# Kernel optimization log

Hardware: AMD Instinct MI355X
Metric: run time of the kernel (lower is better)

Reference implementation:

```python
import jax, jax.numpy as jnp
import numpy as np

D_MODEL = 1024
N_HEAD = 16
B, C, S = 4, 4, 1024


def setup_inputs() -> dict:
    key = jax.random.key(0)
    ks = jax.random.split(key, 5)
    d = D_MODEL
    x = jax.random.normal(ks[0], (B, C, S, d), dtype=jnp.float32)
    scale = 1.0 / np.sqrt(d).astype(np.float32)

    def lin(k):
        return jax.random.normal(k, (d, d), dtype=jnp.float32) * scale

    return {
        "x": x,
        "wq": lin(ks[1]), "bq": jnp.zeros((d,), jnp.float32),
        "wk": lin(ks[2]), "bk": jnp.zeros((d,), jnp.float32),
        "wv": lin(ks[3]), "bv": jnp.zeros((d,), jnp.float32),
        "wo": lin(ks[4]), "bo": jnp.zeros((d,), jnp.float32),
    }


def reference(x, wq, bq, wk, bk, wv, bv, wo, bo):
    b, c, s, d = x.shape
    dh = d // N_HEAD
    nh = N_HEAD * c  # channels folded into heads, as in torch .view

    def proj(w, bias):
        # nn.Linear: y = x @ w.T + b  (w stored as [out, in])
        y = jnp.einsum('bcsd,ed->bcse', x, w) + bias
        # view(B, -1, n_head*C, d_head).transpose(1, 2) -> (B, nh, S, dh)
        return jnp.swapaxes(y.reshape(b, -1, nh, dh), 1, 2)

    # NOTE: original multiplies query by sqrt(d_head) (kept faithfully)
    q = proj(wq, bq) * jnp.sqrt(jnp.asarray(dh, x.dtype))
    k = proj(wk, bk)
    v = proj(wv, bv)

    attn = jax.nn.softmax(jnp.einsum('bhqd,bhkd->bhqk', q, k), axis=-1)
    o = jnp.einsum('bhqk,bhkd->bhqd', attn, v)          # (B, nh, S, dh)
    o = jnp.swapaxes(o, 1, 2).reshape(b, -1, N_HEAD * dh)  # (B, S*C, d)
    o = jnp.einsum('bnd,ed->bne', o, wo) + bo
    return o.reshape(b, c, -1, d)  # (B, C, S, d)
```

## Files before the change

kernel.cpp:

```cpp
#include <hip/hip_runtime.h>
#include <stdint.h>

typedef unsigned short u16;
typedef _Float16 f16;
typedef __attribute__((ext_vector_type(8))) _Float16 f16x8;
typedef __attribute__((ext_vector_type(4))) float f32x4;

__device__ __forceinline__ float exp2fast(float x) {
  return __builtin_amdgcn_exp2f(x);
}

__device__ __forceinline__ f32x4 mfma16(f16x8 a, f16x8 b, f32x4 c) {
  return __builtin_amdgcn_mfma_f32_16x16x32_f16(a, b, c, 0, 0, 0);
}

__device__ __forceinline__ u16 f2h(float f) {
  return __builtin_bit_cast(u16, (f16)f);
}

__device__ __forceinline__ void gld16(const void* g, void* l) {
  __builtin_amdgcn_global_load_lds(
      (const __attribute__((address_space(1))) unsigned int*)g,
      (__attribute__((address_space(3))) unsigned int*)l,
      16, 0, 0);
}

__global__ __launch_bounds__(256) void cvt_f32_f16(const float* __restrict__ in,
                                                   u16* __restrict__ out, int n4) {
  int stride = gridDim.x * blockDim.x;
  for (int i = blockIdx.x * blockDim.x + threadIdx.x; i < n4; i += stride) {
    float4 v = reinterpret_cast<const float4*>(in)[i];
    ushort4 o;
    o.x = f2h(v.x); o.y = f2h(v.y); o.z = f2h(v.z); o.w = f2h(v.w);
    reinterpret_cast<ushort4*>(out)[i] = o;
  }
}

struct Ptr8 {
  const float *s0, *s1, *s2, *s3;
  u16 *d0, *d1, *d2, *d3;
};
__global__ __launch_bounds__(256) void cvt4_f32_f16(Ptr8 p, int n4) {
  const float* in = (blockIdx.y == 0) ? p.s0 : (blockIdx.y == 1) ? p.s1
                    : (blockIdx.y == 2) ? p.s2 : p.s3;
  u16* out = (blockIdx.y == 0) ? p.d0 : (blockIdx.y == 1) ? p.d1
             : (blockIdx.y == 2) ? p.d2 : p.d3;
  int stride = gridDim.x * blockDim.x;
  for (int i = blockIdx.x * blockDim.x + threadIdx.x; i < n4; i += stride) {
    float4 v = reinterpret_cast<const float4*>(in)[i];
    ushort4 o;
    o.x = f2h(v.x); o.y = f2h(v.y); o.z = f2h(v.z); o.w = f2h(v.w);
    reinterpret_cast<ushort4*>(out)[i] = o;
  }
}

__device__ __forceinline__ void stage64(const u16* __restrict__ M, int r0, int k0,
                                        u16* S, int wid, int lane) {
  const int l8 = lane >> 3;
  const int col = k0 + (((lane & 7) ^ l8) << 3);
#pragma unroll
  for (int it = 0; it < 4; ++it) {
    const int rowbase = wid * 32 + it * 8;
    gld16(M + (size_t)(r0 + rowbase + l8) * 1024 + col, S + rowbase * 64);
  }
}

__global__ __launch_bounds__(256) void proj_qkv(
    const u16* __restrict__ xb,
    const u16* __restrict__ wqh, const u16* __restrict__ wkh, const u16* __restrict__ wvh,
    const float* __restrict__ bq, const float* __restrict__ bk, const float* __restrict__ bv,
    u16* __restrict__ Qf, u16* __restrict__ Kf, u16* __restrict__ Vt) {
  const int mat = blockIdx.z;
  const u16* __restrict__ w = (mat == 0) ? wqh : (mat == 1) ? wkh : wvh;
  const float* __restrict__ bias = (mat == 0) ? bq : (mat == 1) ? bk : bv;
  const int m0 = blockIdx.x * 128;
  const int n0 = blockIdx.y * 128;

  __shared__ __align__(16) u16 As[128 * 64];
  __shared__ __align__(16) u16 Bs[128 * 64];

  const int tid = threadIdx.x;
  const int lane = tid & 63;
  const int wid = tid >> 6;
  const int wr = wid >> 1, wc = wid & 1;
  const int qd = lane >> 4, lm = lane & 15;

  f32x4 acc[4][4];
#pragma unroll
  for (int i = 0; i < 4; ++i)
#pragma unroll
    for (int j = 0; j < 4; ++j) acc[i][j] = (f32x4){0.f, 0.f, 0.f, 0.f};

  stage64(xb, m0, 0, As, wid, lane);
  stage64(w, n0, 0, Bs, wid, lane);

  for (int kt = 0; kt < 16; ++kt) {
    __syncthreads();
#pragma unroll
    for (int ks = 0; ks < 2; ++ks) {
      const int gofs = ((ks * 4 + qd) ^ (lm & 7)) << 3;
      f16x8 af[4], bf[4];
#pragma unroll
      for (int i = 0; i < 4; ++i)
        af[i] = *reinterpret_cast<const f16x8*>(As + (wr * 64 + i * 16 + lm) * 64 + gofs);
#pragma unroll
      for (int j = 0; j < 4; ++j)
        bf[j] = *reinterpret_cast<const f16x8*>(Bs + (wc * 64 + j * 16 + lm) * 64 + gofs);
#pragma unroll
      for (int i = 0; i < 4; ++i)
#pragma unroll
        for (int j = 0; j < 4; ++j)
          acc[i][j] = mfma16(af[i], bf[j], acc[i][j]);
    }
    __syncthreads();
    if (kt + 1 < 16) {
      stage64(xb, m0, (kt + 1) * 64, As, wid, lane);
      stage64(w, n0, (kt + 1) * 64, Bs, wid, lane);
    }
  }

  const float scale = (mat == 0) ? 11.5415603f : 1.0f;
#pragma unroll
  for (int i = 0; i < 4; ++i) {
#pragma unroll
    for (int r = 0; r < 4; ++r) {
      int R = m0 + wr * 64 + i * 16 + qd * 4 + r;
      int bb = R >> 12, n = R & 4095;
      int cc = n >> 10, s = n & 1023;
      int rb = s & 3, t = s >> 2;
      int m = cc * 256 + t;
#pragma unroll
      for (int j = 0; j < 4; ++j) {
        int e = n0 + wc * 64 + j * 16 + lm;
        int head = e >> 6, jj = e & 63;
        int h = rb * 16 + head;
        float val = (acc[i][j][r] + bias[e]) * scale;
        u16 hv = f2h(val);
        if (mat == 2) {
          Vt[(((size_t)bb * 64 + h) * 64 + jj) * 1024 + m] = hv;
        } else {
          size_t idx = (((size_t)bb * 64 + h) * 1024 + m) * 64 + jj;
          if (mat == 0) Qf[idx] = hv;
          else          Kf[idx] = hv;
        }
      }
    }
  }
}

__device__ __forceinline__ f16x8 lds_frag(const u16* base, int row, int blk) {
  return *reinterpret_cast<const f16x8*>(base + row * 64 + ((blk ^ (row & 7)) << 3));
}

__device__ __forceinline__ void stage_kv(const u16* __restrict__ Kh,
                                         const u16* __restrict__ Vh, int kc,
                                         u16* KsB, u16* VsB, int wv, int lane) {
  const int l8 = lane >> 3, sl = lane & 7;
  const int rb = wv * 16;
#pragma unroll
  for (int it = 0; it < 2; ++it) {
    int row = rb + it * 8 + l8;
    int gsl = sl ^ l8;
    gld16(Kh + (size_t)(kc * 64 + row) * 64 + gsl * 8, KsB + (rb + it * 8) * 64);
    gld16(Vh + (size_t)row * 1024 + kc * 64 + gsl * 8, VsB + (rb + it * 8) * 64);
  }
}

__global__ __launch_bounds__(256) void attn_kernel(
    const u16* __restrict__ Qf, const u16* __restrict__ Kf,
    const u16* __restrict__ Vt, u16* __restrict__ Of) {
  const int wgid = (blockIdx.x & 7) * 256 + (blockIdx.x >> 3);
  const int bh = wgid >> 3;
  const int m0 = (wgid & 7) * 128;
  const int b = bh >> 6, h = bh & 63;
  const int tid = threadIdx.x, lane = tid & 63, wv = tid >> 6;
  const int qd = lane >> 4, lm = lane & 15;

  __shared__ __align__(16) u16 Ks[2][64 * 64];
  __shared__ __align__(16) u16 Vs[2][64 * 64];

  const size_t hb = (size_t)(b * 64 + h);
  const u16* __restrict__ Qh = Qf + hb * 65536;
  const u16* __restrict__ Kh = Kf + hb * 65536;
  const u16* __restrict__ Vh = Vt + hb * 65536;

  f16x8 qf[2][2];
#pragma unroll
  for (int im = 0; im < 2; ++im)
#pragma unroll
    for (int ks = 0; ks < 2; ++ks)
      qf[im][ks] = *reinterpret_cast<const f16x8*>(
          Qh + (size_t)(m0 + wv * 32 + im * 16 + lm) * 64 + ks * 32 + qd * 8);

  f32x4 oa[2][4];
  float mrow[2] = {-1e30f, -1e30f};
  float lrow[2] = {0.f, 0.f};
#pragma unroll
  for (int im = 0; im < 2; ++im)
#pragma unroll
    for (int jf = 0; jf < 4; ++jf) oa[im][jf] = (f32x4){0.f, 0.f, 0.f, 0.f};

  stage_kv(Kh, Vh, 0, &Ks[0][0], &Vs[0][0], wv, lane);

  for (int kc = 0; kc < 16; ++kc) {
    const int buf = kc & 1;
    __syncthreads();
    if (kc + 1 < 16) stage_kv(Kh, Vh, kc + 1, &Ks[buf ^ 1][0], &Vs[buf ^ 1][0], wv, lane);

    f32x4 sc[2][4];
#pragma unroll
    for (int im = 0; im < 2; ++im)
#pragma unroll
      for (int nf = 0; nf < 4; ++nf) sc[im][nf] = (f32x4){0.f, 0.f, 0.f, 0.f};
    __builtin_amdgcn_s_setprio(1);
#pragma unroll
    for (int ks = 0; ks < 2; ++ks) {
      f16x8 kfr[4];
#pragma unroll
      for (int nf = 0; nf < 4; ++nf)
        kfr[nf] = lds_frag(&Ks[buf][0], nf * 16 + lm, ks * 4 + qd);
#pragma unroll
      for (int im = 0; im < 2; ++im)
#pragma unroll
        for (int nf = 0; nf < 4; ++nf)
          sc[im][nf] = mfma16(kfr[nf], qf[im][ks], sc[im][nf]);
    }
    __builtin_amdgcn_s_setprio(0);

    unsigned int pk[2][8];
#pragma unroll
    for (int im = 0; im < 2; ++im) {
      float pm = sc[im][0][0];
#pragma unroll
      for (int nf = 0; nf < 4; ++nf)
#pragma unroll
        for (int r = 0; r < 4; ++r) pm = fmaxf(pm, sc[im][nf][r]);
      pm = fmaxf(pm, __shfl_xor(pm, 16));
      pm = fmaxf(pm, __shfl_xor(pm, 32));
      if (__all(pm <= mrow[im] + 8.0f)) {
        float mn = mrow[im];
        float s = 0.f;
#pragma unroll
        for (int nf = 0; nf < 4; ++nf) {
          float p0 = exp2fast(sc[im][nf][0] - mn);
          float p1 = exp2fast(sc[im][nf][1] - mn);
          float p2 = exp2fast(sc[im][nf][2] - mn);
          float p3 = exp2fast(sc[im][nf][3] - mn);
          s += (p0 + p1) + (p2 + p3);
          pk[im][2 * nf + 0] = __builtin_bit_cast(unsigned int, __builtin_amdgcn_cvt_pkrtz(p0, p1));
          pk[im][2 * nf + 1] = __builtin_bit_cast(unsigned int, __builtin_amdgcn_cvt_pkrtz(p2, p3));
        }
        s += __shfl_xor(s, 16);
        s += __shfl_xor(s, 32);
        lrow[im] += s;
      } else {
        float mn = fmaxf(mrow[im], pm);
        float corr = exp2fast(mrow[im] - mn);
        mrow[im] = mn;
        float s = 0.f;
#pragma unroll
        for (int nf = 0; nf < 4; ++nf) {
          float p0 = exp2fast(sc[im][nf][0] - mn);
          float p1 = exp2fast(sc[im][nf][1] - mn);
          float p2 = exp2fast(sc[im][nf][2] - mn);
          float p3 = exp2fast(sc[im][nf][3] - mn);
          s += (p0 + p1) + (p2 + p3);
          pk[im][2 * nf + 0] = __builtin_bit_cast(unsigned int, __builtin_amdgcn_cvt_pkrtz(p0, p1));
          pk[im][2 * nf + 1] = __builtin_bit_cast(unsigned int, __builtin_amdgcn_cvt_pkrtz(p2, p3));
        }
        s += __shfl_xor(s, 16);
        s += __shfl_xor(s, 32);
        lrow[im] = lrow[im] * corr + s;
#pragma unroll
        for (int r = 0; r < 4; ++r) {
          float cb = __shfl(corr, qd * 4 + r);
#pragma unroll
          for (int jf = 0; jf < 4; ++jf) oa[im][jf][r] *= cb;
        }
      }
    }

#pragma unroll
    for (int ks = 0; ks < 2; ++ks) {
      f16x8 vfr[4];
#pragma unroll
      for (int jf = 0; jf < 4; ++jf)
        vfr[jf] = lds_frag(&Vs[buf][0], jf * 16 + lm, ks * 4 + qd);
#pragma unroll
      for (int im = 0; im < 2; ++im) {
        union { unsigned int w[4]; f16x8 hv; } pa;
#pragma unroll
        for (int w = 0; w < 4; ++w) {
          int srcl = (((2 * qd + (w >> 1)) & 3) << 4) + lm;
          unsigned int a0 = __shfl(pk[im][2 * (2 * ks + 0) + (w & 1)], srcl);
          unsigned int a1 = __shfl(pk[im][2 * (2 * ks + 1) + (w & 1)], srcl);
          pa.w[w] = (qd & 2) ? a1 : a0;
        }
        __builtin_amdgcn_s_setprio(1);
#pragma unroll
        for (int jf = 0; jf < 4; ++jf)
          oa[im][jf] = mfma16(pa.hv, vfr[jf], oa[im][jf]);
        __builtin_amdgcn_s_setprio(0);
      }
    }
  }

  const int rb = h >> 4, head = h & 15;
#pragma unroll
  for (int im = 0; im < 2; ++im) {
#pragma unroll
    for (int r = 0; r < 4; ++r) {
      float lb = __shfl(lrow[im], qd * 4 + r);
      float inv = 1.0f / lb;
      int mq = m0 + wv * 32 + im * 16 + qd * 4 + r;
      int c = mq >> 8, t = mq & 255;
      int s = t * 4 + rb;
      int n = c * 1024 + s;
#pragma unroll
      for (int jf = 0; jf < 4; ++jf) {
        int j = jf * 16 + lm;
        int f = head * 64 + j;
        Of[((size_t)b * 4096 + n) * 1024 + f] = f2h(oa[im][jf][r] * inv);
      }
    }
  }
}

__global__ __launch_bounds__(256) void out_gemm(
    const u16* __restrict__ Of, const u16* __restrict__ woh,
    const float* __restrict__ bo, float* __restrict__ out) {
  const int m0 = blockIdx.x * 128;
  const int n0 = blockIdx.y * 128;

  __shared__ __align__(16) u16 As[128 * 64];
  __shared__ __align__(16) u16 Bs[128 * 64];

  const int tid = threadIdx.x;
  const int lane = tid & 63;
  const int wid = tid >> 6;
  const int wr = wid >> 1, wc = wid & 1;
  const int qd = lane >> 4, lm = lane & 15;

  f32x4 acc[4][4];
#pragma unroll
  for (int i = 0; i < 4; ++i)
#pragma unroll
    for (int j = 0; j < 4; ++j) acc[i][j] = (f32x4){0.f, 0.f, 0.f, 0.f};

  stage64(Of, m0, 0, As, wid, lane);
  stage64(woh, n0, 0, Bs, wid, lane);

  for (int kt = 0; kt < 16; ++kt) {
    __syncthreads();
#pragma unroll
    for (int ks = 0; ks < 2; ++ks) {
      const int gofs = ((ks * 4 + qd) ^ (lm & 7)) << 3;
      f16x8 af[4], bf[4];
#pragma unroll
      for (int i = 0; i < 4; ++i)
        af[i] = *reinterpret_cast<const f16x8*>(As + (wr * 64 + i * 16 + lm) * 64 + gofs);
#pragma unroll
      for (int j = 0; j < 4; ++j)
        bf[j] = *reinterpret_cast<const f16x8*>(Bs + (wc * 64 + j * 16 + lm) * 64 + gofs);
#pragma unroll
      for (int i = 0; i < 4; ++i)
#pragma unroll
        for (int j = 0; j < 4; ++j)
          acc[i][j] = mfma16(af[i], bf[j], acc[i][j]);
    }
    __syncthreads();
    if (kt + 1 < 16) {
      stage64(Of, m0, (kt + 1) * 64, As, wid, lane);
      stage64(woh, n0, (kt + 1) * 64, Bs, wid, lane);
    }
  }

#pragma unroll
  for (int i = 0; i < 4; ++i) {
#pragma unroll
    for (int r = 0; r < 4; ++r) {
      int R = m0 + wr * 64 + i * 16 + qd * 4 + r;
#pragma unroll
      for (int j = 0; j < 4; ++j) {
        int e = n0 + wc * 64 + j * 16 + lm;
        out[(size_t)R * 1024 + e] = acc[i][j][r] + bo[e];
      }
    }
  }
}

extern "C" void kernel_launch(void* const* d_in, const int* in_sizes, int n_in,
                              void* d_out, int out_size, void* d_ws, size_t ws_size,
                              hipStream_t stream) {
  const float* x  = (const float*)d_in[0];
  const float* wq = (const float*)d_in[1];
  const float* bq = (const float*)d_in[2];
  const float* wk = (const float*)d_in[3];
  const float* bk = (const float*)d_in[4];
  const float* wv = (const float*)d_in[5];
  const float* bv = (const float*)d_in[6];
  const float* wo = (const float*)d_in[7];
  const float* bo = (const float*)d_in[8];
  float* out = (float*)d_out;

  char* ws = (char*)d_ws;
  u16* xb  = (u16*)(ws + 0);
  u16* wqh = (u16*)(ws + 33554432);
  u16* wkh = (u16*)(ws + 35651584);
  u16* wvh = (u16*)(ws + 37748736);
  u16* woh = (u16*)(ws + 39845888);
  u16* Qfb = (u16*)(ws + 41943040);
  u16* Kfb = (u16*)(ws + 75497472);
  u16* Vtb = (u16*)(ws + 109051904);
  u16* Ofb = (u16*)(ws + 142606336);

  cvt_f32_f16<<<4096, 256, 0, stream>>>(x, xb, 16777216 / 4);
  Ptr8 p { wq, wk, wv, wo, wqh, wkh, wvh, woh };
  cvt4_f32_f16<<<dim3(256, 4), 256, 0, stream>>>(p, 1048576 / 4);

  proj_qkv<<<dim3(128, 8, 3), 256, 0, stream>>>(xb, wqh, wkh, wvh, bq, bk, bv,
                                                Qfb, Kfb, Vtb);
  attn_kernel<<<2048, 256, 0, stream>>>(Qfb, Kfb, Vtb, Ofb);
  out_gemm<<<dim3(128, 8), 256, 0, stream>>>(Ofb, woh, bo, out);
}
```

Before: 384.4 us.

## Triple-buffer GEMM LDS staging with K=32 tiles and vmcnt-based barriers

The projection and output GEMMs move from a single-buffered K=64 tile loop, with two __syncthreads per step, to a three-stage ring of K=32 tiles. Each stage is issued two steps ahead through global_load_lds and waited on with s_waitcnt vmcnt plus a single barrier. The goal is to overlap global-to-LDS loads with MFMA work instead of stalling at each barrier. In exchange, shared memory use grows from 32KB to 48KB per block, which may lower occupancy, and the LDS swizzle changes to fit the new row width.

```diff
diff --git a/kernel.cpp b/kernel.cpp
--- a/kernel.cpp
+++ b/kernel.cpp
@@ -24,6 +24,8 @@
       (__attribute__((address_space(3))) unsigned int*)l,
       16, 0, 0);
 }
+
+#define WAITBAR(N) asm volatile("s_waitcnt vmcnt(" #N ")\n\ts_barrier" ::: "memory")
 
 __global__ __launch_bounds__(256) void cvt_f32_f16(const float* __restrict__ in,
                                                    u16* __restrict__ out, int n4) {
@@ -54,15 +56,12 @@
   }
 }
 
-__device__ __forceinline__ void stage64(const u16* __restrict__ M, int r0, int k0,
+__device__ __forceinline__ void stage32(const u16* __restrict__ M, int r0, int k0,
                                         u16* S, int wid, int lane) {
-  const int l8 = lane >> 3;
-  const int col = k0 + (((lane & 7) ^ l8) << 3);
-#pragma unroll
-  for (int it = 0; it < 4; ++it) {
-    const int rowbase = wid * 32 + it * 8;
-    gld16(M + (size_t)(r0 + rowbase + l8) * 1024 + col, S + rowbase * 64);
-  }
+  const int gr = (((lane & 3) ^ ((lane >> 3) & 3)) << 3);
+  const int row = wid * 32 + (lane >> 2);
+  gld16(M + (size_t)(r0 + row) * 1024 + k0 + gr, S + wid * 1024);
+  gld16(M + (size_t)(r0 + row + 16) * 1024 + k0 + gr, S + wid * 1024 + 512);
 }
 
 __global__ __launch_bounds__(256) void proj_qkv(
@@ -76,14 +75,15 @@
   const int m0 = blockIdx.x * 128;
   const int n0 = blockIdx.y * 128;
 
-  __shared__ __align__(16) u16 As[128 * 64];
-  __shared__ __align__(16) u16 Bs[128 * 64];
+  __shared__ __align__(16) u16 As[3 * 4096];
+  __shared__ __align__(16) u16 Bs[3 * 4096];
 
   const int tid = threadIdx.x;
   const int lane = tid & 63;
   const int wid = tid >> 6;
   const int wr = wid >> 1, wc = wid & 1;
   const int qd = lane >> 4, lm = lane & 15;
+  const int rg = (qd ^ ((lm >> 1) & 3)) << 3;
 
   f32x4 acc[4][4];
 #pragma unroll
@@ -91,32 +91,37 @@
 #pragma unroll
     for (int j = 0; j < 4; ++j) acc[i][j] = (f32x4){0.f, 0.f, 0.f, 0.f};
 
-  stage64(xb, m0, 0, As, wid, lane);
-  stage64(w, n0, 0, Bs, wid, lane);
-
-  for (int kt = 0; kt < 16; ++kt) {
-    __syncthreads();
-#pragma unroll
-    for (int ks = 0; ks < 2; ++ks) {
-      const int gofs = ((ks * 4 + qd) ^ (lm & 7)) << 3;
-      f16x8 af[4], bf[4];
-#pragma unroll
-      for (int i = 0; i < 4; ++i)
-        af[i] = *reinterpret_cast<const f16x8*>(As + (wr * 64 + i * 16 + lm) * 64 + gofs);
+  stage32(xb, m0, 0, As, wid, lane);
+  stage32(w, n0, 0, Bs, wid, lane);
+  stage32(xb, m0, 32, As + 4096, wid, lane);
+  stage32(w, n0, 32, Bs + 4096, wid, lane);
+
+  int cur = 0;
+  for (int t = 0; t < 32; ++t) {
+    if (t < 31) WAITBAR(4); else WAITBAR(0);
+
+    if (t + 2 < 32) {
+      int nb = cur + 2; if (nb >= 3) nb -= 3;
+      stage32(xb, m0, (t + 2) * 32, As + nb * 4096, wid, lane);
+      stage32(w, n0, (t + 2) * 32, Bs + nb * 4096, wid, lane);
+    }
+
+    const u16* aB = As + cur * 4096;
+    const u16* bB = Bs + cur * 4096;
+    f16x8 af[4], bf[4];
+#pragma unroll
+    for (int i = 0; i < 4; ++i)
+      af[i] = *reinterpret_cast<const f16x8*>(aB + (wr * 64 + i * 16 + lm) * 32 + rg);
+#pragma unroll
+    for (int j = 0; j < 4; ++j)
+      bf[j] = *reinterpret_cast<const f16x8*>(bB + (wc * 64 + j * 16 + lm) * 32 + rg);
+#pragma unroll
+    for (int i = 0; i < 4; ++i)
 #pragma unroll
       for (int j = 0; j < 4; ++j)
-        bf[j] = *reinterpret_cast<const f16x8*>(Bs + (wc * 64 + j * 16 + lm) * 64 + gofs);
-#pragma unroll
-      for (int i = 0; i < 4; ++i)
-#pragma unroll
-        for (int j = 0; j < 4; ++j)
-          acc[i][j] = mfma16(af[i], bf[j], acc[i][j]);
-    }
-    __syncthreads();
-    if (kt + 1 < 16) {
-      stage64(xb, m0, (kt + 1) * 64, As, wid, lane);
-      stage64(w, n0, (kt + 1) * 64, Bs, wid, lane);
-    }
+        acc[i][j] = mfma16(af[i], bf[j], acc[i][j]);
+
+    ++cur; if (cur == 3) cur = 0;
   }
 
   const float scale = (mat == 0) ? 11.5415603f : 1.0f;
@@ -332,14 +337,15 @@
   const int m0 = blockIdx.x * 128;
   const int n0 = blockIdx.y * 128;
 
-  __shared__ __align__(16) u16 As[128 * 64];
-  __shared__ __align__(16) u16 Bs[128 * 64];
+  __shared__ __align__(16) u16 As[3 * 4096];
+  __shared__ __align__(16) u16 Bs[3 * 4096];
 
   const int tid = threadIdx.x;
   const int lane = tid & 63;
   const int wid = tid >> 6;
   const int wr = wid >> 1, wc = wid & 1;
   const int qd = lane >> 4, lm = lane & 15;
+  const int rg = (qd ^ ((lm >> 1) & 3)) << 3;
 
   f32x4 acc[4][4];
 #pragma unroll
@@ -347,32 +353,34 @@
 #pragma unroll
     for (int j = 0; j < 4; ++j) acc[i][j] = (f32x4){0.f, 0.f, 0.f, 0.f};
 
-  stage64(Of, m0, 0, As, wid, lane);
-  stage64(woh, n0, 0, Bs, wid, lane);
-
-  for (int kt = 0; kt < 16; ++kt) {
-    __syncthreads();
-#pragma unroll
-    for (int ks = 0; ks < 2; ++ks) {
-      const int gofs = ((ks * 4 + qd) ^ (lm & 7)) << 3;
-      f16x8 af[4], bf[4];
-#pragma unroll
-      for (int i = 0; i < 4; ++i)
-        af[i] = *reinterpret_cast<const f16x8*>(As + (wr * 64 + i * 16 + lm) * 64 + gofs);
+  stage32(Of, m0, 0, As, wid, lane);
+  stage32(woh, n0, 0, Bs, wid, lane);
+  stage32(Of, m0, 32, As + 4096, wid, lane);
+  stage32(woh, n0, 32, Bs + 4096, wid, lane);
+
+  int cur = 0;
+  for (int t = 0; t < 32; ++t) {
+    if (t < 31) WAITBAR(4); else WAITBAR(0);
+    if (t + 2 < 32) {
+      int nb = cur + 2; if (nb >= 3) nb -= 3;
+      stage32(Of, m0, (t + 2) * 32, As + nb * 4096, wid, lane);
+      stage32(woh, n0, (t + 2) * 32, Bs + nb * 4096, wid, lane);
+    }
+    const u16* aB = As + cur * 4096;
+    const u16* bB = Bs + cur * 4096;
+    f16x8 af[4], bf[4];
+#pragma unroll
+    for (int i = 0; i < 4; ++i)
+      af[i] = *reinterpret_cast<const f16x8*>(aB + (wr * 64 + i * 16 + lm) * 32 + rg);
+#pragma unroll
+    for (int j = 0; j < 4; ++j)
+      bf[j] = *reinterpret_cast<const f16x8*>(bB + (wc * 64 + j * 16 + lm) * 32 + rg);
+#pragma unroll
+    for (int i = 0; i < 4; ++i)
 #pragma unroll
       for (int j = 0; j < 4; ++j)
-        bf[j] = *reinterpret_cast<const f16x8*>(Bs + (wc * 64 + j * 16 + lm) * 64 + gofs);
-#pragma unroll
-      for (int i = 0; i < 4; ++i)
-#pragma unroll
-        for (int j = 0; j < 4; ++j)
-          acc[i][j] = mfma16(af[i], bf[j], acc[i][j]);
-    }
-    __syncthreads();
-    if (kt + 1 < 16) {
-      stage64(Of, m0, (kt + 1) * 64, As, wid, lane);
-      stage64(woh, n0, (kt + 1) * 64, Bs, wid, lane);
-    }
+        acc[i][j] = mfma16(af[i], bf[j], acc[i][j]);
+    ++cur; if (cur == 3) cur = 0;
   }
 
 #pragma unroll
```

After: 399.6 us. 1.04x slower.

## Fuse Q/K/V projections into one block sharing the staged x tile

Applied to the files above, without the earlier changes.

Each QKV projection block now computes all three outputs (Q, K, V) for its tile. The x tile in LDS is loaded once and reused across three weight tiles, which removes two of every three loads of x and cuts the grid from 3072 to 1024 blocks. In exchange, each thread holds three times as many accumulators (192 floats) and each block uses 64KB of LDS. That can reduce occupancy or cause register spills, and fewer blocks means less parallelism across the CUs.

```diff
diff --git a/kernel.cpp b/kernel.cpp
--- a/kernel.cpp
+++ b/kernel.cpp
@@ -70,14 +70,11 @@
     const u16* __restrict__ wqh, const u16* __restrict__ wkh, const u16* __restrict__ wvh,
     const float* __restrict__ bq, const float* __restrict__ bk, const float* __restrict__ bv,
     u16* __restrict__ Qf, u16* __restrict__ Kf, u16* __restrict__ Vt) {
-  const int mat = blockIdx.z;
-  const u16* __restrict__ w = (mat == 0) ? wqh : (mat == 1) ? wkh : wvh;
-  const float* __restrict__ bias = (mat == 0) ? bq : (mat == 1) ? bk : bv;
   const int m0 = blockIdx.x * 128;
   const int n0 = blockIdx.y * 128;
 
   __shared__ __align__(16) u16 As[128 * 64];
-  __shared__ __align__(16) u16 Bs[128 * 64];
+  __shared__ __align__(16) u16 Bs[3][128 * 64];
 
   const int tid = threadIdx.x;
   const int lane = tid & 63;
@@ -85,63 +82,77 @@
   const int wr = wid >> 1, wc = wid & 1;
   const int qd = lane >> 4, lm = lane & 15;
 
-  f32x4 acc[4][4];
-#pragma unroll
-  for (int i = 0; i < 4; ++i)
-#pragma unroll
-    for (int j = 0; j < 4; ++j) acc[i][j] = (f32x4){0.f, 0.f, 0.f, 0.f};
+  f32x4 acc[3][4][4];
+#pragma unroll
+  for (int mt = 0; mt < 3; ++mt)
+#pragma unroll
+    for (int i = 0; i < 4; ++i)
+#pragma unroll
+      for (int j = 0; j < 4; ++j) acc[mt][i][j] = (f32x4){0.f, 0.f, 0.f, 0.f};
 
   stage64(xb, m0, 0, As, wid, lane);
-  stage64(w, n0, 0, Bs, wid, lane);
+  stage64(wqh, n0, 0, Bs[0], wid, lane);
+  stage64(wkh, n0, 0, Bs[1], wid, lane);
+  stage64(wvh, n0, 0, Bs[2], wid, lane);
 
   for (int kt = 0; kt < 16; ++kt) {
     __syncthreads();
 #pragma unroll
     for (int ks = 0; ks < 2; ++ks) {
       const int gofs = ((ks * 4 + qd) ^ (lm & 7)) << 3;
-      f16x8 af[4], bf[4];
+      f16x8 af[4];
 #pragma unroll
       for (int i = 0; i < 4; ++i)
         af[i] = *reinterpret_cast<const f16x8*>(As + (wr * 64 + i * 16 + lm) * 64 + gofs);
 #pragma unroll
-      for (int j = 0; j < 4; ++j)
-        bf[j] = *reinterpret_cast<const f16x8*>(Bs + (wc * 64 + j * 16 + lm) * 64 + gofs);
-#pragma unroll
-      for (int i = 0; i < 4; ++i)
+      for (int mt = 0; mt < 3; ++mt) {
+        f16x8 bf[4];
 #pragma unroll
         for (int j = 0; j < 4; ++j)
-          acc[i][j] = mfma16(af[i], bf[j], acc[i][j]);
+          bf[j] = *reinterpret_cast<const f16x8*>(Bs[mt] + (wc * 64 + j * 16 + lm) * 64 + gofs);
+#pragma unroll
+        for (int i = 0; i < 4; ++i)
+#pragma unroll
+          for (int j = 0; j < 4; ++j)
+            acc[mt][i][j] = mfma16(af[i], bf[j], acc[mt][i][j]);
+      }
     }
     __syncthreads();
     if (kt + 1 < 16) {
       stage64(xb, m0, (kt + 1) * 64, As, wid, lane);
-      stage64(w, n0, (kt + 1) * 64, Bs, wid, lane);
-    }
-  }
-
-  const float scale = (mat == 0) ? 11.5415603f : 1.0f;
-#pragma unroll
-  for (int i = 0; i < 4; ++i) {
-#pragma unroll
-    for (int r = 0; r < 4; ++r) {
-      int R = m0 + wr * 64 + i * 16 + qd * 4 + r;
-      int bb = R >> 12, n = R & 4095;
-      int cc = n >> 10, s = n & 1023;
-      int rb = s & 3, t = s >> 2;
-      int m = cc * 256 + t;
-#pragma unroll
-      for (int j = 0; j < 4; ++j) {
-        int e = n0 + wc * 64 + j * 16 + lm;
-        int head = e >> 6, jj = e & 63;
-        int h = rb * 16 + head;
-        float val = (acc[i][j][r] + bias[e]) * scale;
-        u16 hv = f2h(val);
-        if (mat == 2) {
-          Vt[(((size_t)bb * 64 + h) * 64 + jj) * 1024 + m] = hv;
-        } else {
-          size_t idx = (((size_t)bb * 64 + h) * 1024 + m) * 64 + jj;
-          if (mat == 0) Qf[idx] = hv;
-          else          Kf[idx] = hv;
+      stage64(wqh, n0, (kt + 1) * 64, Bs[0], wid, lane);
+      stage64(wkh, n0, (kt + 1) * 64, Bs[1], wid, lane);
+      stage64(wvh, n0, (kt + 1) * 64, Bs[2], wid, lane);
+    }
+  }
+
+#pragma unroll
+  for (int mt = 0; mt < 3; ++mt) {
+    const float* bias = (mt == 0) ? bq : (mt == 1) ? bk : bv;
+    const float scale = (mt == 0) ? 11.5415603f : 1.0f;
+#pragma unroll
+    for (int i = 0; i < 4; ++i) {
+#pragma unroll
+      for (int r = 0; r < 4; ++r) {
+        int R = m0 + wr * 64 + i * 16 + qd * 4 + r;
+        int bb = R >> 12, n = R & 4095;
+        int cc = n >> 10, s = n & 1023;
+        int rb = s & 3, t = s >> 2;
+        int m = cc * 256 + t;
+#pragma unroll
+        for (int j = 0; j < 4; ++j) {
+          int e = n0 + wc * 64 + j * 16 + lm;
+          int head = e >> 6, jj = e & 63;
+          int h = rb * 16 + head;
+          float val = (acc[mt][i][j][r] + bias[e]) * scale;
+          u16 hv = f2h(val);
+          if (mt == 2) {
+            Vt[(((size_t)bb * 64 + h) * 64 + jj) * 1024 + m] = hv;
+          } else {
+            size_t idx = (((size_t)bb * 64 + h) * 1024 + m) * 64 + jj;
+            if (mt == 0) Qf[idx] = hv;
+            else         Kf[idx] = hv;
+          }
         }
       }
     }
@@ -418,8 +429,8 @@
   Ptr8 p { wq, wk, wv, wo, wqh, wkh, wvh, woh };
   cvt4_f32_f16<<<dim3(256, 4), 256, 0, stream>>>(p, 1048576 / 4);
 
-  proj_qkv<<<dim3(128, 8, 3), 256, 0, stream>>>(xb, wqh, wkh, wvh, bq, bk, bv,
-                                                Qfb, Kfb, Vtb);
+  proj_qkv<<<dim3(128, 8), 256, 0, stream>>>(xb, wqh, wkh, wvh, bq, bk, bv,
+                                             Qfb, Kfb, Vtb);
   attn_kernel<<<2048, 256, 0, stream>>>(Qfb, Kfb, Vtb, Ofb);
   out_gemm<<<dim3(128, 8), 256, 0, stream>>>(Ofb, woh, bo, out);
 }
```

Result: no change. 389.6 us (median of 2 runs) (+1.3%).
